# Optimization experiments

Measured on AMD Instinct MI355X. Metric: run time of the kernel, lower is better.

## Reference

```python
import jax, jax.numpy as jnp
import numpy as np

HS = 512   # hidden_size
IN = 2048  # input_size
MB = 100   # memory_bank_size
T  = 4096  # nImg


def setup_inputs() -> dict:
    key = jax.random.key(0)
    ks = jax.random.split(key, 20)

    def w(k, i, o):
        return jax.random.normal(k, (i, o), jnp.float32) * (1.0 / np.sqrt(i))

    def b(k, o):
        return jax.random.normal(k, (o,), jnp.float32) * 0.01

    return {
        "hidden_out_a": jax.random.normal(ks[0], (T, IN), jnp.float32),
        "hidden_out_m": jax.random.normal(ks[1], (T, IN), jnp.float32),
        "W_ca": w(ks[2], HS + IN, HS),  "b_ca": b(ks[3], HS),    # hidden_to_content_a
        "W_cm": w(ks[4], HS + IN, HS),  "b_cm": b(ks[5], HS),    # hidden_to_content_m
        "W_wp": w(ks[6], 3 * HS, 3),    "b_wp": b(ks[7], 3),     # write_prob
        "W_wpa": w(ks[8], HS + IN, MB), "b_wpa": b(ks[9], MB),   # write_prob_a
        "W_wpm": w(ks[10], HS + IN, MB),"b_wpm": b(ks[11], MB),  # write_prob_m
        "W_rp": w(ks[12], 3 * HS, MB),  "b_rp": b(ks[13], MB),   # read_prob
        "W_rh": w(ks[14], 2 * HS, HS),  "b_rh": b(ks[15], HS),   # read_to_hidden
        "W_rha": w(ks[16], 2 * HS + IN, HS), "b_rha": b(ks[17], HS),  # read_to_hidden_a
        "W_rhm": w(ks[18], 2 * HS + IN, HS), "b_rhm": b(ks[19], HS),  # read_to_hidden_m
        "nImg": T,
    }


def reference(hidden_out_a, hidden_out_m,
              W_ca, b_ca, W_cm, b_cm,
              W_wp, b_wp, W_wpa, b_wpa, W_wpm, b_wpm,
              W_rp, b_rp, W_rh, b_rh,
              W_rha, b_rha, W_rhm, b_rhm,
              nImg):
    hs = W_rh.shape[1]
    mb = W_rp.shape[1]

    def step(carry, xs):
        mem, h, ha, hm = carry            # mem: [MB, HS]; h/ha/hm: [HS]
        xa, xm = xs                       # [IN] each
        xh = jnp.concatenate([ha, hm, h])               # [3*HS]
        ar = jax.nn.softmax(xh @ W_rp + b_rp)           # [MB]
        r = ar @ mem                                    # [HS] memory read
        h1 = jax.nn.relu(jnp.concatenate([r, h]) @ W_rh + b_rh)
        ha1 = jax.nn.relu(jnp.concatenate([xa, r, ha]) @ W_rha + b_rha)
        hm1 = jax.nn.relu(jnp.concatenate([xm, r, hm]) @ W_rhm + b_rhm)
        aw = jax.nn.softmax(xh @ W_wp + b_wp)           # [3] stream gate
        xha = jnp.concatenate([ha, xa])                 # [HS+IN]
        xhm = jnp.concatenate([hm, xm])
        c_a = jax.nn.relu(xha @ W_ca + b_ca)            # [HS]
        c_m = jax.nn.relu(xhm @ W_cm + b_cm)
        aw_a = jax.nn.softmax(xha @ W_wpa + b_wpa)      # [MB]
        aw_m = jax.nn.softmax(xhm @ W_wpm + b_wpm)
        mem = aw[0] * mem + aw[1] * aw_a[:, None] * c_a + aw[2] * aw_m[:, None] * c_m
        return (mem, h1, ha1, hm1), h1

    init = (jnp.zeros((mb, hs), hidden_out_a.dtype),
            jnp.zeros((hs,), hidden_out_a.dtype),
            jnp.zeros((hs,), hidden_out_a.dtype),
            jnp.zeros((hs,), hidden_out_a.dtype))
    _, hiddens = jax.lax.scan(step, init,
                              (hidden_out_a[:nImg], hidden_out_m[:nImg]))
    return hiddens  # [nImg, HS]
```

## Files before the change

kernel.cpp:

```cpp
#include <hip/hip_runtime.h>
#include <cstdint>
#include <cstddef>

#define HS 512

constexpr int TPB  = 512;
constexpr int GBLK = 64;
constexpr int OWNB = 24;
constexpr int WPAD = 516;

constexpr size_t OFF_TWrp  = 0;
constexpr size_t OFF_TWwp  = OFF_TWrp  + 100*1536;
constexpr size_t OFF_TWwpa = OFF_TWwp  + 3*1536;
constexpr size_t OFF_TWwpm = OFF_TWwpa + 100*512;
constexpr size_t OFF_TWca  = OFF_TWwpm + 100*512;
constexpr size_t OFF_TWcm  = OFF_TWca  + 512*512;
constexpr size_t OFF_TWh0  = OFF_TWcm  + 512*512;
constexpr size_t OFF_TWh1  = OFF_TWh0  + 512*512;
constexpr size_t OFF_TWh2  = OFF_TWh1  + 512*512;
constexpr size_t OFF_TWu0  = OFF_TWh2  + 512*512;
constexpr size_t OFF_TWu1  = OFF_TWu0  + 512*512;
constexpr size_t OFF_TWu2  = OFF_TWu1  + 512*512;
constexpr size_t OFF_PAca  = OFF_TWu2  + 512*512;
constexpr size_t OFF_PMcm  = OFF_PAca  + 4096*512;
constexpr size_t OFF_PArha = OFF_PMcm  + 4096*512;
constexpr size_t OFF_PMrhm = OFF_PArha + 4096*512;
constexpr size_t OFF_PAwpa = OFF_PMrhm + 4096*512;
constexpr size_t OFF_PMwpm = OFF_PAwpa + 4096*100;
constexpr size_t OFF_CARRY = OFF_PMwpm + 4096*100;
constexpr size_t OFF_BCAST = OFF_CARRY + 2*1536*2;

__device__ __forceinline__ unsigned long long ald(const unsigned long long* p) {
  return __hip_atomic_load(const_cast<unsigned long long*>(p),
                           __ATOMIC_RELAXED, __HIP_MEMORY_SCOPE_AGENT);
}
__device__ __forceinline__ void gstTag(unsigned long long* p, float v, unsigned tag) {
  unsigned long long u = ((unsigned long long)tag << 32) | (unsigned long long)__float_as_uint(v);
  __hip_atomic_store(p, u, __ATOMIC_RELAXED, __HIP_MEMORY_SCOPE_AGENT);
}
__device__ __forceinline__ float xrsum(float v) {
  #pragma unroll
  for (int o = 32; o; o >>= 1) v += __shfl_xor(v, o, 64);
  return v;
}
__device__ __forceinline__ float rsum16(float v) {
  #pragma unroll
  for (int o = 8; o; o >>= 1) v += __shfl_xor(v, o, 64);
  return v;
}

template<int K4>
__device__ __forceinline__ float dotK(const float* __restrict__ w, const float* x) {
  int l = threadIdx.x & 63;
  const float4* w4 = (const float4*)w;
  const float4* x4 = (const float4*)x;
  float acc = 0.f;
  #pragma unroll
  for (int it = 0; it < K4; ++it) {
    float4 a = w4[l + 64*it];
    float4 b = x4[l + 64*it];
    acc += a.x*b.x + a.y*b.y + a.z*b.z + a.w*b.w;
  }
  return acc;
}

__device__ __forceinline__ float dot16_512(const float* __restrict__ w,
                                           const float* x, int gl) {
  const float4* w4 = (const float4*)w;
  const float4* x4 = (const float4*)x;
  float acc = 0.f;
  #pragma unroll
  for (int it = 0; it < 8; ++it) {
    float4 a = w4[gl + 16*it];
    float4 b = x4[gl + 16*it];
    acc += a.x*b.x + a.y*b.y + a.z*b.z + a.w*b.w;
  }
  return acc;
}

__device__ __forceinline__ void dot16_2x512(const float* __restrict__ w,
                                            const float* xa, const float* xm,
                                            int gl, float& ra, float& rm) {
  const float4* w4 = (const float4*)w;
  const float4* a4 = (const float4*)xa;
  const float4* m4 = (const float4*)xm;
  float sa = 0.f, sm = 0.f;
  #pragma unroll
  for (int it = 0; it < 8; ++it) {
    float4 wv = w4[gl + 16*it], av = a4[gl + 16*it], mv = m4[gl + 16*it];
    sa += wv.x*av.x + wv.y*av.y + wv.z*av.z + wv.w*av.w;
    sm += wv.x*mv.x + wv.y*mv.y + wv.z*mv.z + wv.w*mv.w;
  }
  #pragma unroll
  for (int o = 8; o; o >>= 1) { sa += __shfl_xor(sa, o, 64); sm += __shfl_xor(sm, o, 64); }
  ra = sa; rm = sm;
}

__global__ void initK(unsigned long long* carryT, unsigned long long* bcast) {
  int i = blockIdx.x * blockDim.x + threadIdx.x, st = gridDim.x * blockDim.x;
  for (int k = i; k < 1536; k += st) carryT[k] = (1ull << 32);
  for (int k = i; k < 1536; k += st) carryT[1536 + k] = 0ull;
  for (int k = i; k < 2 * 1344; k += st) bcast[k] = 0ull;
}

__global__ void transK(const float* __restrict__ src, float* __restrict__ dst, int R, int C) {
  __shared__ float tile[32][33];
  int c0 = blockIdx.x * 32, r0 = blockIdx.y * 32;
  for (int i = threadIdx.y; i < 32; i += 8) {
    int r = r0 + i, c = c0 + threadIdx.x;
    tile[i][threadIdx.x] = (r < R && c < C) ? src[(size_t)r * C + c] : 0.f;
  }
  __syncthreads();
  for (int i = threadIdx.y; i < 32; i += 8) {
    int c = c0 + i, r = r0 + threadIdx.x;
    if (c < C && r < R) dst[(size_t)c * R + r] = tile[threadIdx.x][i];
  }
}

__global__ __launch_bounds__(256) void gemmK(const float* __restrict__ X,
                                             const float* __restrict__ W,
                                             float* __restrict__ C, int N) {
  __shared__ float As[16][68];
  __shared__ float Bs[16][68];
  int t0 = blockIdx.y * 64, n0 = blockIdx.x * 64;
  int tid = threadIdx.x, tx = tid & 15, ty = tid >> 4;
  float acc[4][4] = {};
  for (int k0 = 0; k0 < 2048; k0 += 16) {
    {
      int r = tid >> 2, c = (tid & 3) * 4;
      float4 v = *(const float4*)(X + (size_t)(t0 + r) * 2048 + k0 + c);
      As[c + 0][r] = v.x; As[c + 1][r] = v.y; As[c + 2][r] = v.z; As[c + 3][r] = v.w;
    }
    {
      int kr = tid >> 4, c = (tid & 15) * 4;
      int gcol = n0 + c;
      const float* src = W + (size_t)(k0 + kr) * N + gcol;
      #pragma unroll
      for (int i = 0; i < 4; ++i) Bs[kr][c + i] = (gcol + i < N) ? src[i] : 0.f;
    }
    __syncthreads();
    #pragma unroll
    for (int kk = 0; kk < 16; ++kk) {
      float4 a4 = *(const float4*)&As[kk][ty * 4];
      float4 b4 = *(const float4*)&Bs[kk][tx * 4];
      float av[4] = {a4.x, a4.y, a4.z, a4.w};
      float bv[4] = {b4.x, b4.y, b4.z, b4.w};
      #pragma unroll
      for (int i = 0; i < 4; ++i)
        #pragma unroll
        for (int j = 0; j < 4; ++j) acc[i][j] += av[i] * bv[j];
    }
    __syncthreads();
  }
  #pragma unroll
  for (int i = 0; i < 4; ++i)
    #pragma unroll
    for (int j = 0; j < 4; ++j) {
      int col = n0 + tx * 4 + j;
      if (col < N) C[(size_t)(t0 + ty * 4 + i) * N + col] = acc[i][j];
    }
}

__global__ __launch_bounds__(256) void gemm128(const float* __restrict__ X,
                                               const float* __restrict__ W,
                                               float* __restrict__ C) {
  __shared__ float As[8][132];
  __shared__ float Bs[8][132];
  const int N = 512;
  int t0 = blockIdx.y * 128, n0 = blockIdx.x * 128;
  int tid = threadIdx.x, tx = tid & 15, ty = tid >> 4;
  float acc[8][8] = {};
  for (int k0 = 0; k0 < 2048; k0 += 8) {
    int r = tid >> 1, c4 = (tid & 1) * 4;
    float4 va = *(const float4*)(X + (size_t)(t0 + r) * 2048 + k0 + c4);
    int kr = tid >> 5, cb = (tid & 31) * 4;
    float4 vb = *(const float4*)(W + (size_t)(k0 + kr) * N + n0 + cb);
    __syncthreads();
    As[c4 + 0][r] = va.x; As[c4 + 1][r] = va.y; As[c4 + 2][r] = va.z; As[c4 + 3][r] = va.w;
    Bs[kr][cb] = vb.x; Bs[kr][cb + 1] = vb.y; Bs[kr][cb + 2] = vb.z; Bs[kr][cb + 3] = vb.w;
    __syncthreads();
    #pragma unroll
    for (int kk = 0; kk < 8; ++kk) {
      float av[8], bv[8];
      *(float4*)av       = *(const float4*)&As[kk][ty * 8];
      *(float4*)(av + 4) = *(const float4*)&As[kk][ty * 8 + 4];
      *(float4*)bv       = *(const float4*)&Bs[kk][tx * 8];
      *(float4*)(bv + 4) = *(const float4*)&Bs[kk][tx * 8 + 4];
      #pragma unroll
      for (int i = 0; i < 8; ++i)
        #pragma unroll
        for (int j = 0; j < 8; ++j) acc[i][j] += av[i] * bv[j];
    }
  }
  #pragma unroll
  for (int i = 0; i < 8; ++i) {
    float* dst = C + (size_t)(t0 + ty * 8 + i) * N + n0 + tx * 8;
    *(float4*)dst       = *(float4*)&acc[i][0];
    *(float4*)(dst + 4) = *(float4*)&acc[i][4];
  }
}

struct RArgs {
  const float *TWrp, *TWwp, *TWwpa, *TWwpm, *TWca, *TWcm;
  const float *TWh0, *TWh1, *TWh2, *TWu0, *TWu1, *TWu2;
  const float *PAca, *PMcm, *PArha, *PMrhm, *PAwpa, *PMwpm;
  const float *b_ca, *b_cm, *b_wp, *b_wpa, *b_wpm, *b_rp, *b_rh, *b_rha, *b_rhm;
  unsigned long long *carryT, *bcast;
  float *out;
  int nT;
};

__global__ __launch_bounds__(TPB, 1) void recurK(RArgs a) {
  const int tid  = threadIdx.x;
  const int lane = tid & 63;
  const int lw   = tid >> 6;
  const int g    = tid >> 4;
  const int gl   = tid & 15;
  const int b    = blockIdx.x;

  __shared__ __align__(16) float s_wca[8 * WPAD];
  __shared__ __align__(16) float s_wcm[8 * WPAD];
  __shared__ __align__(16) float s_wbig[2 * 1536];
  __shared__ __align__(16) float s_wsm[4 * WPAD];
  __shared__ __align__(16) float s_TWu[OWNB * WPAD];
  __shared__ __align__(16) float s_G[OWNB * 112];
  __shared__ __align__(16) float s_x[1536];
  __shared__ __align__(16) float s_c[1024];
  __shared__ float s_ar[112], s_awa[112], s_awm[112], s_aw[4];

  const int r0a = (b + 51) & 63;
  const int r1m = (b + 25) & 63;
  const bool big1_grp = (b < 36);
  const bool big1_wp  = (b >= 40 && b <= 42);

  for (int i = tid; i < 8 * WPAD; i += TPB) {
    int row = i / WPAD, col = i - row * WPAD;
    if (col < 512) {
      s_wca[i] = a.TWca[(size_t)(b * 8 + row) * 512 + col];
      s_wcm[i] = a.TWcm[(size_t)(b * 8 + row) * 512 + col];
    }
  }
  for (int i = tid; i < 1536; i += TPB) {
    s_wbig[i] = a.TWrp[(size_t)b * 1536 + i];
    float v2 = 0.f;
    if (big1_grp)      v2 = a.TWrp[(size_t)(b + 64) * 1536 + i];
    else if (big1_wp)  v2 = a.TWwp[(size_t)(b - 40) * 1536 + i];
    s_wbig[1536 + i] = v2;
  }
  for (int i = tid; i < 4 * WPAD; i += TPB) {
    int sl = i / WPAD, col = i - sl * WPAD;
    float v = 0.f;
    if (col < 512) {
      if (sl == 0)      v = a.TWwpa[(size_t)r0a * 512 + col];
      else if (sl == 1) v = (r0a < 36) ? a.TWwpa[(size_t)(r0a + 64) * 512 + col] : 0.f;
      else if (sl == 2) v = a.TWwpm[(size_t)r1m * 512 + col];
      else              v = (r1m < 36) ? a.TWwpm[(size_t)(r1m + 64) * 512 + col] : 0.f;
    }
    s_wsm[i] = v;
  }
  for (int i = tid; i < OWNB * WPAD; i += TPB) {
    int rr = i / WPAD, col = i - rr * WPAD;
    if (col < 512) {
      int q = b * OWNB + rr, hsel = q >> 9, j = q & 511;
      const float* src = (hsel == 0) ? a.TWu0 : (hsel == 1) ? a.TWu1 : a.TWu2;
      s_TWu[i] = src[(size_t)j * 512 + col];
    }
  }
  for (int i = tid; i < OWNB * 112; i += TPB) s_G[i] = 0.f;
  if (tid < 112) { s_ar[tid] = 0.f; s_awa[tid] = 0.f; s_awm[tid] = 0.f; }

  int dstA = -1, xoffA = 0, strideA = 512, rowA = 0;
  float biasA = 0.f;
  const float* preAPtr = nullptr;
  if (lw < 2) {
    int col = b * 8 + g; rowA = g;
    dstA = col; biasA = a.b_ca[col]; preAPtr = a.PAca + col;
  } else if (lw < 4) {
    int col = b * 8 + (g - 8); rowA = g - 8;
    dstA = 512 + col; biasA = a.b_cm[col]; preAPtr = a.PMcm + col;
  } else if (lw == 4) {
    int sl = g - 16;
    if (sl == 0)                  { rowA = 0; dstA = 1124 + r0a;      biasA = a.b_wpa[r0a];      preAPtr = a.PAwpa + r0a;      xoffA = 0;   strideA = 100; }
    else if (sl == 1 && r0a < 36) { rowA = 1; dstA = 1124 + r0a + 64; biasA = a.b_wpa[r0a + 64]; preAPtr = a.PAwpa + r0a + 64; xoffA = 0;   strideA = 100; }
    else if (sl == 2)             { rowA = 2; dstA = 1224 + r1m;      biasA = a.b_wpm[r1m];      preAPtr = a.PMwpm + r1m;      xoffA = 512; strideA = 100; }
    else if (sl == 3 && r1m < 36) { rowA = 3; dstA = 1224 + r1m + 64; biasA = a.b_wpm[r1m + 64]; preAPtr = a.PMwpm + r1m + 64; xoffA = 512; strideA = 100; }
  }
  int dstBig = -1, bigOff = 0;
  float biasBig = 0.f;
  if (lw == 6) { dstBig = 1024 + b; biasBig = a.b_rp[b]; bigOff = 0; }
  else if (lw == 7) {
    if (big1_grp)      { dstBig = 1024 + b + 64;  biasBig = a.b_rp[b + 64]; bigOff = 1536; }
    else if (big1_wp)  { dstBig = 1324 + (b - 40); biasBig = a.b_wp[b - 40]; bigOff = 1536; }
  }
  int ownHsel = 0, ownJ = 0, whXo = 0;
  float biasO = 0.f;
  const float* preOPtr = nullptr;
  const float* whPtr = nullptr;
  if (g < OWNB) {
    int q = b * OWNB + g, hsel = q >> 9, j = q & 511;
    ownHsel = hsel; ownJ = j;
    if (hsel == 0)      { biasO = a.b_rh[j];                           whPtr = a.TWh0 + (size_t)j * 512; whXo = 1024; }
    else if (hsel == 1) { biasO = a.b_rha[j]; preOPtr = a.PArha + j;   whPtr = a.TWh1 + (size_t)j * 512; whXo = 0; }
    else                { biasO = a.b_rhm[j]; preOPtr = a.PMrhm + j;   whPtr = a.TWh2 + (size_t)j * 512; whXo = 512; }
  }
  __syncthreads();

  float preA_c = preAPtr ? preAPtr[0] : 0.f;
  float preO_c = preOPtr ? preOPtr[0] : 0.f;

  float whv = 0.f;
  for (int t = 0; t < a.nT; ++t) {
    const unsigned tagB = (unsigned)t + 1;
    unsigned long long* bc = a.bcast + (size_t)(t & 1) * 1344;

    {
      const unsigned long long* cin = a.carryT + (size_t)(t & 1) * 1536;
      int i0 = tid, i1 = tid + 512, i2 = tid + 1024;
      unsigned long long v0 = ald(cin + i0), v1 = ald(cin + i1), v2 = ald(cin + i2);
      while (((unsigned)(v0 >> 32) < tagB) | ((unsigned)(v1 >> 32) < tagB) |
             ((unsigned)(v2 >> 32) < tagB)) {
        __builtin_amdgcn_s_sleep(1);
        v0 = ald(cin + i0); v1 = ald(cin + i1); v2 = ald(cin + i2);
      }
      s_x[i0] = __uint_as_float((unsigned)v0);
      s_x[i1] = __uint_as_float((unsigned)v1);
      s_x[i2] = __uint_as_float((unsigned)v2);
    }
    __syncthreads();

    const int tn = (t + 1 < a.nT) ? t + 1 : t;
    float preA_n = preAPtr ? preAPtr[(size_t)tn * strideA] : 0.f;
    float preO_n = preOPtr ? preOPtr[(size_t)tn * 512] : 0.f;

    if (lw < 2) {
      float v = rsum16(dot16_512(s_wca + rowA * WPAD, s_x, gl));
      if (!gl) gstTag(bc + dstA, fmaxf(v + preA_c + biasA, 0.f), tagB);
    } else if (lw < 4) {
      float v = rsum16(dot16_512(s_wcm + rowA * WPAD, s_x + 512, gl));
      if (!gl) gstTag(bc + dstA, fmaxf(v + preA_c + biasA, 0.f), tagB);
    } else if (lw == 4) {
      if (dstA >= 0) {
        float v = rsum16(dot16_512(s_wsm + rowA * WPAD, s_x + xoffA, gl));
        if (!gl) gstTag(bc + dstA, v + preA_c + biasA, tagB);
      }
    } else if (lw >= 6) {
      if (dstBig >= 0) {
        float v = xrsum(dotK<6>(s_wbig + bigOff, s_x));
        if (!lane) gstTag(bc + dstBig, v + biasBig, tagB);
      }
    }
    if (g < OWNB) whv = rsum16(dot16_512(whPtr, s_x + whXo, gl));

    if (lw < 3) {
      int base = 1024 + lw * 100;
      const unsigned long long* p1 = bc + base + lane;
      bool two = lane < 36;
      unsigned long long v1 = ald(p1);
      unsigned long long v2 = two ? ald(p1 + 64) : ~0ull;
      while (((unsigned)(v1 >> 32) < tagB) | ((unsigned)(v2 >> 32) < tagB)) {
        __builtin_amdgcn_s_sleep(1);
        v1 = ald(p1); if (two) v2 = ald(p1 + 64);
      }
      float x1 = __uint_as_float((unsigned)v1);
      float x2 = two ? __uint_as_float((unsigned)v2) : -3.0e38f;
      float m = fmaxf(x1, x2);
      #pragma unroll
      for (int o = 32; o; o >>= 1) m = fmaxf(m, __shfl_xor(m, o, 64));
      float e1 = expf(x1 - m);
      float e2 = two ? expf(x2 - m) : 0.f;
      float ss = e1 + e2;
      #pragma unroll
      for (int o = 32; o; o >>= 1) ss += __shfl_xor(ss, o, 64);
      float inv = 1.f / ss;
      float* dst = (lw == 0) ? s_ar : (lw == 1) ? s_awa : s_awm;
      dst[lane] = e1 * inv;
      if (two) dst[64 + lane] = e2 * inv;
    } else if (lw == 3) {
      float x = -3.0e38f;
      if (lane < 3) {
        const unsigned long long* p = bc + 1324 + lane;
        unsigned long long v = ald(p);
        while ((unsigned)(v >> 32) < tagB) { __builtin_amdgcn_s_sleep(1); v = ald(p); }
        x = __uint_as_float((unsigned)v);
      }
      float m = x;
      #pragma unroll
      for (int o = 32; o; o >>= 1) m = fmaxf(m, __shfl_xor(m, o, 64));
      float e = (lane < 3) ? expf(x - m) : 0.f;
      float ss = e;
      #pragma unroll
      for (int o = 32; o; o >>= 1) ss += __shfl_xor(ss, o, 64);
      if (lane < 3) s_aw[lane] = e / ss;
    } else {
      int base = tid - 256;
      const unsigned long long* p = bc + base;
      unsigned long long v0 = ald(p), v1 = ald(p + 256), v2 = ald(p + 512), v3 = ald(p + 768);
      while (((unsigned)(v0 >> 32) < tagB) | ((unsigned)(v1 >> 32) < tagB) |
             ((unsigned)(v2 >> 32) < tagB) | ((unsigned)(v3 >> 32) < tagB)) {
        __builtin_amdgcn_s_sleep(1);
        v0 = ald(p); v1 = ald(p + 256); v2 = ald(p + 512); v3 = ald(p + 768);
      }
      s_c[base]       = __uint_as_float((unsigned)v0);
      s_c[base + 256] = __uint_as_float((unsigned)v1);
      s_c[base + 512] = __uint_as_float((unsigned)v2);
      s_c[base + 768] = __uint_as_float((unsigned)v3);
    }
    __syncthreads();

    unsigned long long* cout = a.carryT + (size_t)((t + 1) & 1) * 1536;
    if (g < OWNB) {
      const float aw0 = s_aw[0], aw1 = s_aw[1], aw2 = s_aw[2];
      float uA, uM;
      dot16_2x512(s_TWu + (size_t)g * WPAD, s_c, s_c + 512, gl, uA, uM);

      float* grow = s_G + g * 112;
      float gv[7];
      float contrib = 0.f;
      #pragma unroll
      for (int k = 0; k < 7; ++k) {
        int idx = gl + 16 * k;
        gv[k] = grow[idx];
        contrib += s_ar[idx] * gv[k];
      }
      contrib = rsum16(contrib);
      if (!gl) {
        float h = fmaxf(contrib + whv + preO_c + biasO, 0.f);
        if (ownHsel == 0) {
          a.out[(size_t)t * 512 + ownJ] = h;
          gstTag(cout + 1024 + ownJ, h, tagB + 1);
        } else if (ownHsel == 1) {
          gstTag(cout + ownJ, h, tagB + 1);
        } else {
          gstTag(cout + 512 + ownJ, h, tagB + 1);
        }
      }
      #pragma unroll
      for (int k = 0; k < 7; ++k) {
        int idx = gl + 16 * k;
        grow[idx] = aw0 * gv[k] + aw1 * s_awa[idx] * uA + aw2 * s_awm[idx] * uM;
      }
    }

    preA_c = preA_n;
    preO_c = preO_n;
  }
}

extern "C" void kernel_launch(void* const* d_in, const int* in_sizes, int n_in,
                              void* d_out, int out_size, void* d_ws, size_t ws_size,
                              hipStream_t stream) {
  const float* Xa    = (const float*)d_in[0];
  const float* Xm    = (const float*)d_in[1];
  const float* W_ca  = (const float*)d_in[2];  const float* b_ca  = (const float*)d_in[3];
  const float* W_cm  = (const float*)d_in[4];  const float* b_cm  = (const float*)d_in[5];
  const float* W_wp  = (const float*)d_in[6];  const float* b_wp  = (const float*)d_in[7];
  const float* W_wpa = (const float*)d_in[8];  const float* b_wpa = (const float*)d_in[9];
  const float* W_wpm = (const float*)d_in[10]; const float* b_wpm = (const float*)d_in[11];
  const float* W_rp  = (const float*)d_in[12]; const float* b_rp  = (const float*)d_in[13];
  const float* W_rh  = (const float*)d_in[14]; const float* b_rh  = (const float*)d_in[15];
  const float* W_rha = (const float*)d_in[16]; const float* b_rha = (const float*)d_in[17];
  const float* W_rhm = (const float*)d_in[18]; const float* b_rhm = (const float*)d_in[19];

  int nT = out_size / HS;
  float* ws = (float*)d_ws;

  initK<<<dim3(64), dim3(256), 0, stream>>>(
      (unsigned long long*)(ws + OFF_CARRY),
      (unsigned long long*)(ws + OFF_BCAST));

  dim3 tb(32, 8);
  auto tg = [](int R, int C) { return dim3((C + 31) / 32, (R + 31) / 32); };
  transK<<<tg(1536, 100), tb, 0, stream>>>(W_rp,                       ws + OFF_TWrp,  1536, 100);
  transK<<<tg(1536, 3),   tb, 0, stream>>>(W_wp,                       ws + OFF_TWwp,  1536, 3);
  transK<<<tg(512, 100),  tb, 0, stream>>>(W_wpa,                      ws + OFF_TWwpa, 512, 100);
  transK<<<tg(512, 100),  tb, 0, stream>>>(W_wpm,                      ws + OFF_TWwpm, 512, 100);
  transK<<<tg(512, 512),  tb, 0, stream>>>(W_ca,                       ws + OFF_TWca,  512, 512);
  transK<<<tg(512, 512),  tb, 0, stream>>>(W_cm,                       ws + OFF_TWcm,  512, 512);
  transK<<<tg(512, 512),  tb, 0, stream>>>(W_rh  + 512 * 512,          ws + OFF_TWh0,  512, 512);
  transK<<<tg(512, 512),  tb, 0, stream>>>(W_rha + (size_t)2560 * 512, ws + OFF_TWh1,  512, 512);
  transK<<<tg(512, 512),  tb, 0, stream>>>(W_rhm + (size_t)2560 * 512, ws + OFF_TWh2,  512, 512);
  transK<<<tg(512, 512),  tb, 0, stream>>>(W_rh,                       ws + OFF_TWu0,  512, 512);
  transK<<<tg(512, 512),  tb, 0, stream>>>(W_rha + (size_t)2048 * 512, ws + OFF_TWu1,  512, 512);
  transK<<<tg(512, 512),  tb, 0, stream>>>(W_rhm + (size_t)2048 * 512, ws + OFF_TWu2,  512, 512);

  int tB = nT / 128;
  gemm128<<<dim3(4, tB), dim3(256), 0, stream>>>(Xa, W_ca + (size_t)512 * 512, ws + OFF_PAca);
  gemm128<<<dim3(4, tB), dim3(256), 0, stream>>>(Xm, W_cm + (size_t)512 * 512, ws + OFF_PMcm);
  gemm128<<<dim3(4, tB), dim3(256), 0, stream>>>(Xa, W_rha,                    ws + OFF_PArha);
  gemm128<<<dim3(4, tB), dim3(256), 0, stream>>>(Xm, W_rhm,                    ws + OFF_PMrhm);
  int tB64 = nT / 64;
  gemmK<<<dim3(2, tB64), dim3(256), 0, stream>>>(Xa, W_wpa + (size_t)512 * 100, ws + OFF_PAwpa, 100);
  gemmK<<<dim3(2, tB64), dim3(256), 0, stream>>>(Xm, W_wpm + (size_t)512 * 100, ws + OFF_PMwpm, 100);

  RArgs a;
  a.TWrp  = ws + OFF_TWrp;  a.TWwp  = ws + OFF_TWwp;
  a.TWwpa = ws + OFF_TWwpa; a.TWwpm = ws + OFF_TWwpm;
  a.TWca  = ws + OFF_TWca;  a.TWcm  = ws + OFF_TWcm;
  a.TWh0  = ws + OFF_TWh0;  a.TWh1  = ws + OFF_TWh1;  a.TWh2 = ws + OFF_TWh2;
  a.TWu0  = ws + OFF_TWu0;  a.TWu1  = ws + OFF_TWu1;  a.TWu2 = ws + OFF_TWu2;
  a.PAca  = ws + OFF_PAca;  a.PMcm  = ws + OFF_PMcm;
  a.PArha = ws + OFF_PArha; a.PMrhm = ws + OFF_PMrhm;
  a.PAwpa = ws + OFF_PAwpa; a.PMwpm = ws + OFF_PMwpm;
  a.b_ca = b_ca; a.b_cm = b_cm; a.b_wp = b_wp; a.b_wpa = b_wpa; a.b_wpm = b_wpm;
  a.b_rp = b_rp; a.b_rh = b_rh; a.b_rha = b_rha; a.b_rhm = b_rhm;
  a.carryT = (unsigned long long*)(ws + OFF_CARRY);
  a.bcast  = (unsigned long long*)(ws + OFF_BCAST);
  a.out    = (float*)d_out;
  a.nT     = nT;

  recurK<<<dim3(GBLK), dim3(TPB), 0, stream>>>(a);
}
```

Baseline: 24.60 ms.

## Keep per-thread weight slices and memory state in registers instead of LDS

Moves every thread's weight slices (content, write-prob, read-prob, Wh and U rows) out of shared-memory staging and into float4 register arrays loaded once before the recurrent loop. The per-row memory projection state G also moves from shared memory into a per-thread register array. This removes repeated LDS reads of weights on every timestep of the latency-bound recurrence, leaving LDS traffic only for the broadcast inputs. In exchange it raises VGPR pressure by roughly 100+ registers per thread, with some risk of spills at 512 threads per block.

```diff
diff --git a/kernel.cpp b/kernel.cpp
--- a/kernel.cpp
+++ b/kernel.cpp
@@ -7,7 +7,6 @@
 constexpr int TPB  = 512;
 constexpr int GBLK = 64;
 constexpr int OWNB = 24;
-constexpr int WPAD = 516;
 
 constexpr size_t OFF_TWrp  = 0;
 constexpr size_t OFF_TWwp  = OFF_TWrp  + 100*1536;
@@ -49,53 +48,6 @@
   return v;
 }
 
-template<int K4>
-__device__ __forceinline__ float dotK(const float* __restrict__ w, const float* x) {
-  int l = threadIdx.x & 63;
-  const float4* w4 = (const float4*)w;
-  const float4* x4 = (const float4*)x;
-  float acc = 0.f;
-  #pragma unroll
-  for (int it = 0; it < K4; ++it) {
-    float4 a = w4[l + 64*it];
-    float4 b = x4[l + 64*it];
-    acc += a.x*b.x + a.y*b.y + a.z*b.z + a.w*b.w;
-  }
-  return acc;
-}
-
-__device__ __forceinline__ float dot16_512(const float* __restrict__ w,
-                                           const float* x, int gl) {
-  const float4* w4 = (const float4*)w;
-  const float4* x4 = (const float4*)x;
-  float acc = 0.f;
-  #pragma unroll
-  for (int it = 0; it < 8; ++it) {
-    float4 a = w4[gl + 16*it];
-    float4 b = x4[gl + 16*it];
-    acc += a.x*b.x + a.y*b.y + a.z*b.z + a.w*b.w;
-  }
-  return acc;
-}
-
-__device__ __forceinline__ void dot16_2x512(const float* __restrict__ w,
-                                            const float* xa, const float* xm,
-                                            int gl, float& ra, float& rm) {
-  const float4* w4 = (const float4*)w;
-  const float4* a4 = (const float4*)xa;
-  const float4* m4 = (const float4*)xm;
-  float sa = 0.f, sm = 0.f;
-  #pragma unroll
-  for (int it = 0; it < 8; ++it) {
-    float4 wv = w4[gl + 16*it], av = a4[gl + 16*it], mv = m4[gl + 16*it];
-    sa += wv.x*av.x + wv.y*av.y + wv.z*av.z + wv.w*av.w;
-    sm += wv.x*mv.x + wv.y*mv.y + wv.z*mv.z + wv.w*mv.w;
-  }
-  #pragma unroll
-  for (int o = 8; o; o >>= 1) { sa += __shfl_xor(sa, o, 64); sm += __shfl_xor(sm, o, 64); }
-  ra = sa; rm = sm;
-}
-
 __global__ void initK(unsigned long long* carryT, unsigned long long* bcast) {
   int i = blockIdx.x * blockDim.x + threadIdx.x, st = gridDim.x * blockDim.x;
   for (int k = i; k < 1536; k += st) carryT[k] = (1ull << 32);
@@ -218,12 +170,6 @@
   const int gl   = tid & 15;
   const int b    = blockIdx.x;
 
-  __shared__ __align__(16) float s_wca[8 * WPAD];
-  __shared__ __align__(16) float s_wcm[8 * WPAD];
-  __shared__ __align__(16) float s_wbig[2 * 1536];
-  __shared__ __align__(16) float s_wsm[4 * WPAD];
-  __shared__ __align__(16) float s_TWu[OWNB * WPAD];
-  __shared__ __align__(16) float s_G[OWNB * 112];
   __shared__ __align__(16) float s_x[1536];
   __shared__ __align__(16) float s_c[1024];
   __shared__ float s_ar[112], s_awa[112], s_awm[112], s_aw[4];
@@ -233,75 +179,84 @@
   const bool big1_grp = (b < 36);
   const bool big1_wp  = (b >= 40 && b <= 42);
 
-  for (int i = tid; i < 8 * WPAD; i += TPB) {
-    int row = i / WPAD, col = i - row * WPAD;
-    if (col < 512) {
-      s_wca[i] = a.TWca[(size_t)(b * 8 + row) * 512 + col];
-      s_wcm[i] = a.TWcm[(size_t)(b * 8 + row) * 512 + col];
-    }
-  }
-  for (int i = tid; i < 1536; i += TPB) {
-    s_wbig[i] = a.TWrp[(size_t)b * 1536 + i];
-    float v2 = 0.f;
-    if (big1_grp)      v2 = a.TWrp[(size_t)(b + 64) * 1536 + i];
-    else if (big1_wp)  v2 = a.TWwp[(size_t)(b - 40) * 1536 + i];
-    s_wbig[1536 + i] = v2;
-  }
-  for (int i = tid; i < 4 * WPAD; i += TPB) {
-    int sl = i / WPAD, col = i - sl * WPAD;
-    float v = 0.f;
-    if (col < 512) {
-      if (sl == 0)      v = a.TWwpa[(size_t)r0a * 512 + col];
-      else if (sl == 1) v = (r0a < 36) ? a.TWwpa[(size_t)(r0a + 64) * 512 + col] : 0.f;
-      else if (sl == 2) v = a.TWwpm[(size_t)r1m * 512 + col];
-      else              v = (r1m < 36) ? a.TWwpm[(size_t)(r1m + 64) * 512 + col] : 0.f;
-    }
-    s_wsm[i] = v;
-  }
-  for (int i = tid; i < OWNB * WPAD; i += TPB) {
-    int rr = i / WPAD, col = i - rr * WPAD;
-    if (col < 512) {
-      int q = b * OWNB + rr, hsel = q >> 9, j = q & 511;
-      const float* src = (hsel == 0) ? a.TWu0 : (hsel == 1) ? a.TWu1 : a.TWu2;
-      s_TWu[i] = src[(size_t)j * 512 + col];
-    }
-  }
-  for (int i = tid; i < OWNB * 112; i += TPB) s_G[i] = 0.f;
   if (tid < 112) { s_ar[tid] = 0.f; s_awa[tid] = 0.f; s_awm[tid] = 0.f; }
 
-  int dstA = -1, xoffA = 0, strideA = 512, rowA = 0;
+  int dstA = -1, xoffA = 0, strideA = 512;
+  bool reluA = false;
   float biasA = 0.f;
   const float* preAPtr = nullptr;
+  const float* wARow = nullptr;
   if (lw < 2) {
-    int col = b * 8 + g; rowA = g;
-    dstA = col; biasA = a.b_ca[col]; preAPtr = a.PAca + col;
+    int col = b * 8 + g;
+    dstA = col; reluA = true; biasA = a.b_ca[col]; preAPtr = a.PAca + col;
+    wARow = a.TWca + (size_t)col * 512; xoffA = 0;
   } else if (lw < 4) {
-    int col = b * 8 + (g - 8); rowA = g - 8;
-    dstA = 512 + col; biasA = a.b_cm[col]; preAPtr = a.PMcm + col;
+    int col = b * 8 + (g - 8);
+    dstA = 512 + col; reluA = true; biasA = a.b_cm[col]; preAPtr = a.PMcm + col;
+    wARow = a.TWcm + (size_t)col * 512; xoffA = 512;
   } else if (lw == 4) {
     int sl = g - 16;
-    if (sl == 0)                  { rowA = 0; dstA = 1124 + r0a;      biasA = a.b_wpa[r0a];      preAPtr = a.PAwpa + r0a;      xoffA = 0;   strideA = 100; }
-    else if (sl == 1 && r0a < 36) { rowA = 1; dstA = 1124 + r0a + 64; biasA = a.b_wpa[r0a + 64]; preAPtr = a.PAwpa + r0a + 64; xoffA = 0;   strideA = 100; }
-    else if (sl == 2)             { rowA = 2; dstA = 1224 + r1m;      biasA = a.b_wpm[r1m];      preAPtr = a.PMwpm + r1m;      xoffA = 512; strideA = 100; }
-    else if (sl == 3 && r1m < 36) { rowA = 3; dstA = 1224 + r1m + 64; biasA = a.b_wpm[r1m + 64]; preAPtr = a.PMwpm + r1m + 64; xoffA = 512; strideA = 100; }
-  }
-  int dstBig = -1, bigOff = 0;
+    strideA = 100;
+    if (sl == 0)                  { dstA = 1124 + r0a;      biasA = a.b_wpa[r0a];      preAPtr = a.PAwpa + r0a;      wARow = a.TWwpa + (size_t)r0a * 512;        xoffA = 0;   }
+    else if (sl == 1 && r0a < 36) { dstA = 1124 + r0a + 64; biasA = a.b_wpa[r0a + 64]; preAPtr = a.PAwpa + r0a + 64; wARow = a.TWwpa + (size_t)(r0a + 64) * 512; xoffA = 0;   }
+    else if (sl == 2)             { dstA = 1224 + r1m;      biasA = a.b_wpm[r1m];      preAPtr = a.PMwpm + r1m;      wARow = a.TWwpm + (size_t)r1m * 512;        xoffA = 512; }
+    else if (sl == 3 && r1m < 36) { dstA = 1224 + r1m + 64; biasA = a.b_wpm[r1m + 64]; preAPtr = a.PMwpm + r1m + 64; wARow = a.TWwpm + (size_t)(r1m + 64) * 512; xoffA = 512; }
+  }
+  int dstBig = -1;
   float biasBig = 0.f;
-  if (lw == 6) { dstBig = 1024 + b; biasBig = a.b_rp[b]; bigOff = 0; }
+  const float* wBigRow = nullptr;
+  if (lw == 6) { dstBig = 1024 + b; biasBig = a.b_rp[b]; wBigRow = a.TWrp + (size_t)b * 1536; }
   else if (lw == 7) {
-    if (big1_grp)      { dstBig = 1024 + b + 64;  biasBig = a.b_rp[b + 64]; bigOff = 1536; }
-    else if (big1_wp)  { dstBig = 1324 + (b - 40); biasBig = a.b_wp[b - 40]; bigOff = 1536; }
-  }
+    if (big1_grp)      { dstBig = 1024 + b + 64;   biasBig = a.b_rp[b + 64]; wBigRow = a.TWrp + (size_t)(b + 64) * 1536; }
+    else if (big1_wp)  { dstBig = 1324 + (b - 40); biasBig = a.b_wp[b - 40]; wBigRow = a.TWwp + (size_t)(b - 40) * 1536; }
+  }
+  const bool own = (g < OWNB);
   int ownHsel = 0, ownJ = 0, whXo = 0;
   float biasO = 0.f;
   const float* preOPtr = nullptr;
-  const float* whPtr = nullptr;
-  if (g < OWNB) {
+  const float* whRow = nullptr;
+  const float* uRow = nullptr;
+  if (own) {
     int q = b * OWNB + g, hsel = q >> 9, j = q & 511;
     ownHsel = hsel; ownJ = j;
-    if (hsel == 0)      { biasO = a.b_rh[j];                           whPtr = a.TWh0 + (size_t)j * 512; whXo = 1024; }
-    else if (hsel == 1) { biasO = a.b_rha[j]; preOPtr = a.PArha + j;   whPtr = a.TWh1 + (size_t)j * 512; whXo = 0; }
-    else                { biasO = a.b_rhm[j]; preOPtr = a.PMrhm + j;   whPtr = a.TWh2 + (size_t)j * 512; whXo = 512; }
+    if (hsel == 0)      { biasO = a.b_rh[j];
+                          whRow = a.TWh0 + (size_t)j * 512; whXo = 1024;
+                          uRow  = a.TWu0 + (size_t)j * 512; }
+    else if (hsel == 1) { biasO = a.b_rha[j]; preOPtr = a.PArha + j;
+                          whRow = a.TWh1 + (size_t)j * 512; whXo = 0;
+                          uRow  = a.TWu1 + (size_t)j * 512; }
+    else                { biasO = a.b_rhm[j]; preOPtr = a.PMrhm + j;
+                          whRow = a.TWh2 + (size_t)j * 512; whXo = 512;
+                          uRow  = a.TWu2 + (size_t)j * 512; }
+  }
+
+  float4 wA[8];
+  float4 wU[8];
+  float4 wWh[8];
+  float4 wB[6];
+  float  gr[7];
+  #pragma unroll
+  for (int it = 0; it < 8; ++it) wA[it] = wU[it] = wWh[it] = make_float4(0.f, 0.f, 0.f, 0.f);
+  #pragma unroll
+  for (int it = 0; it < 6; ++it) wB[it] = make_float4(0.f, 0.f, 0.f, 0.f);
+  #pragma unroll
+  for (int k = 0; k < 7; ++k) gr[k] = 0.f;
+
+  if (wARow) {
+    const float4* w4 = (const float4*)wARow;
+    #pragma unroll
+    for (int it = 0; it < 8; ++it) wA[it] = w4[gl + 16 * it];
+  }
+  if (own) {
+    const float4* u4 = (const float4*)uRow;
+    const float4* h4 = (const float4*)whRow;
+    #pragma unroll
+    for (int it = 0; it < 8; ++it) { wU[it] = u4[gl + 16 * it]; wWh[it] = h4[gl + 16 * it]; }
+  }
+  if (wBigRow) {
+    const float4* w4 = (const float4*)wBigRow;
+    #pragma unroll
+    for (int it = 0; it < 6; ++it) wB[it] = w4[lane + 64 * it];
   }
   __syncthreads();
 
@@ -332,24 +287,41 @@
     float preA_n = preAPtr ? preAPtr[(size_t)tn * strideA] : 0.f;
     float preO_n = preOPtr ? preOPtr[(size_t)tn * 512] : 0.f;
 
-    if (lw < 2) {
-      float v = rsum16(dot16_512(s_wca + rowA * WPAD, s_x, gl));
-      if (!gl) gstTag(bc + dstA, fmaxf(v + preA_c + biasA, 0.f), tagB);
-    } else if (lw < 4) {
-      float v = rsum16(dot16_512(s_wcm + rowA * WPAD, s_x + 512, gl));
-      if (!gl) gstTag(bc + dstA, fmaxf(v + preA_c + biasA, 0.f), tagB);
-    } else if (lw == 4) {
-      if (dstA >= 0) {
-        float v = rsum16(dot16_512(s_wsm + rowA * WPAD, s_x + xoffA, gl));
-        if (!gl) gstTag(bc + dstA, v + preA_c + biasA, tagB);
-      }
-    } else if (lw >= 6) {
-      if (dstBig >= 0) {
-        float v = xrsum(dotK<6>(s_wbig + bigOff, s_x));
-        if (!lane) gstTag(bc + dstBig, v + biasBig, tagB);
-      }
-    }
-    if (g < OWNB) whv = rsum16(dot16_512(whPtr, s_x + whXo, gl));
+    if (dstA >= 0) {
+      const float4* x4 = (const float4*)(s_x + xoffA);
+      float acc = 0.f;
+      #pragma unroll
+      for (int it = 0; it < 8; ++it) {
+        float4 xv = x4[gl + 16 * it];
+        acc += wA[it].x * xv.x + wA[it].y * xv.y + wA[it].z * xv.z + wA[it].w * xv.w;
+      }
+      float v = rsum16(acc);
+      if (!gl) {
+        v += preA_c + biasA;
+        if (reluA) v = fmaxf(v, 0.f);
+        gstTag(bc + dstA, v, tagB);
+      }
+    } else if (dstBig >= 0) {
+      const float4* x4 = (const float4*)s_x;
+      float acc = 0.f;
+      #pragma unroll
+      for (int it = 0; it < 6; ++it) {
+        float4 xv = x4[lane + 64 * it];
+        acc += wB[it].x * xv.x + wB[it].y * xv.y + wB[it].z * xv.z + wB[it].w * xv.w;
+      }
+      float v = xrsum(acc);
+      if (!lane) gstTag(bc + dstBig, v + biasBig, tagB);
+    }
+    if (own) {
+      const float4* x4 = (const float4*)(s_x + whXo);
+      float acc = 0.f;
+      #pragma unroll
+      for (int it = 0; it < 8; ++it) {
+        float4 xv = x4[gl + 16 * it];
+        acc += wWh[it].x * xv.x + wWh[it].y * xv.y + wWh[it].z * xv.z + wWh[it].w * xv.w;
+      }
+      whv = rsum16(acc);
+    }
 
     if (lw < 3) {
       int base = 1024 + lw * 100;
@@ -408,20 +380,24 @@
     __syncthreads();
 
     unsigned long long* cout = a.carryT + (size_t)((t + 1) & 1) * 1536;
-    if (g < OWNB) {
+    if (own) {
       const float aw0 = s_aw[0], aw1 = s_aw[1], aw2 = s_aw[2];
-      float uA, uM;
-      dot16_2x512(s_TWu + (size_t)g * WPAD, s_c, s_c + 512, gl, uA, uM);
-
-      float* grow = s_G + g * 112;
-      float gv[7];
+      const float4* a4 = (const float4*)s_c;
+      const float4* m4 = (const float4*)(s_c + 512);
+      float sa = 0.f, sm = 0.f;
+      #pragma unroll
+      for (int it = 0; it < 8; ++it) {
+        float4 av = a4[gl + 16 * it], mv = m4[gl + 16 * it];
+        sa += wU[it].x * av.x + wU[it].y * av.y + wU[it].z * av.z + wU[it].w * av.w;
+        sm += wU[it].x * mv.x + wU[it].y * mv.y + wU[it].z * mv.z + wU[it].w * mv.w;
+      }
+      #pragma unroll
+      for (int o = 8; o; o >>= 1) { sa += __shfl_xor(sa, o, 64); sm += __shfl_xor(sm, o, 64); }
+      const float uA = sa, uM = sm;
+
       float contrib = 0.f;
       #pragma unroll
-      for (int k = 0; k < 7; ++k) {
-        int idx = gl + 16 * k;
-        gv[k] = grow[idx];
-        contrib += s_ar[idx] * gv[k];
-      }
+      for (int k = 0; k < 7; ++k) contrib += s_ar[gl + 16 * k] * gr[k];
       contrib = rsum16(contrib);
       if (!gl) {
         float h = fmaxf(contrib + whv + preO_c + biasO, 0.f);
@@ -437,7 +413,7 @@
       #pragma unroll
       for (int k = 0; k < 7; ++k) {
         int idx = gl + 16 * k;
-        grow[idx] = aw0 * gv[k] + aw1 * s_awa[idx] * uA + aw2 * s_awm[idx] * uM;
+        gr[k] = aw0 * gr[k] + aw1 * s_awa[idx] * uA + aw2 * s_awm[idx] * uM;
       }
     }
 
```

Result: faster. 22.80 ms, median of 2 (-7.3%).
